# Kernel tuning notes

Hardware: AMD Instinct MI355X
Metric: run time of the kernel (lower is better)

Reference implementation:

```python
import jax, jax.numpy as jnp
import numpy as np

SEQLEN, K, OLDK, HEADS = 2048, 1024, 1024, 16
BASE = 10000.0


def rope(x):
    # x: [b, t, K]; RoPENd over 1 channel dim: rotate adjacent pairs
    # pair j at position t rotated by angle t * BASE**(-j/(K/2))
    t = x.shape[1]
    half = K // 2
    theta = 1.0 / (BASE ** (jnp.arange(half, dtype=jnp.float32) / half))  # [half]
    ang = jnp.arange(t, dtype=jnp.float32)[:, None] * theta[None, :]      # [t, half]
    cos, sin = jnp.cos(ang), jnp.sin(ang)
    xr = x.reshape(x.shape[0], t, half, 2)
    xe, xo = xr[..., 0], xr[..., 1]
    re = xe * cos - xo * sin
    im = xe * sin + xo * cos
    return jnp.stack([re, im], axis=-1).reshape(x.shape)


def setup_inputs() -> dict:
    key = jax.random.key(0)
    ks = jax.random.split(key, 5)
    b = 4
    x = jax.random.normal(ks[0], (b, SEQLEN, OLDK), jnp.float32)
    sc_in = 1.0 / np.sqrt(OLDK).astype(np.float32)
    Wq = jax.random.normal(ks[1], (K, OLDK), jnp.float32) * sc_in
    Wk = jax.random.normal(ks[2], (K, OLDK), jnp.float32) * sc_in
    Wv = jax.random.normal(ks[3], (K, OLDK), jnp.float32) * sc_in
    Wu = jax.random.normal(ks[4], (K, K), jnp.float32) * (1.0 / np.sqrt(K).astype(np.float32))
    bu = jnp.zeros((K,), jnp.float32)
    return {"x": x, "Wq": Wq, "Wk": Wk, "Wv": Wv, "Wu": Wu, "bu": bu}


def reference(x, Wq, Wk, Wv, Wu, bu):
    b, t, _ = x.shape
    h = HEADS
    s = K // h  # head dim
    q = rope(x @ Wq.T)   # [b, t, K]
    k = rope(x @ Wk.T)
    v = x @ Wv.T
    # split heads: [b, h, t, s]
    q = q.reshape(b, t, h, s).transpose(0, 2, 1, 3)
    k = k.reshape(b, t, h, s).transpose(0, 2, 1, 3)
    v = v.reshape(b, t, h, s).transpose(0, 2, 1, 3)
    dot = jnp.einsum('bhqd,bhkd->bhqk', q, k) / jnp.sqrt(jnp.float32(s))
    att = jax.nn.softmax(dot, axis=-1)
    out = jnp.einsum('bhqk,bhkd->bhqd', att, v)
    out = out.transpose(0, 2, 1, 3).reshape(b, t, h * s)
    return out @ Wu.T + bu
```

## Files before the change

kernel.cpp:

```cpp
#include <hip/hip_runtime.h>

#define TSEQ 2048
#define KDIM 1024
#define NHEAD 16
#define HDIM 64
#define BATCH 4
#define HALF 512

typedef __attribute__((ext_vector_type(4))) float f32x4;
typedef __attribute__((ext_vector_type(16))) float f32x16;
typedef __attribute__((ext_vector_type(8))) short short8;
typedef __attribute__((ext_vector_type(4))) unsigned short us4;
typedef __attribute__((ext_vector_type(4))) unsigned int u32x4;

#if __has_builtin(__builtin_amdgcn_exp2f)
#define EXP2(x) __builtin_amdgcn_exp2f(x)
#else
#define EXP2(x) __expf((x)*0.6931471805599453f)
#endif

__device__ __forceinline__ unsigned short f2bf(float f){
  unsigned int u = __float_as_uint(f);
  u += 0x7FFFu + ((u >> 16) & 1u);
  return (unsigned short)(u >> 16);
}

__device__ __forceinline__ unsigned int cvtpk(float a, float b){
  unsigned int r;
  asm("v_cvt_pk_bf16_f32 %0, %1, %2" : "=v"(r) : "v"(a), "v"(b));
  return r;
}

__device__ __forceinline__ f32x4 mfma16(short8 a, short8 b, f32x4 c){
  return __builtin_amdgcn_mfma_f32_16x16x32_bf16(a, b, c, 0, 0, 0);
}
__device__ __forceinline__ f32x16 mfma32(short8 a, short8 b, f32x16 c){
  return __builtin_amdgcn_mfma_f32_32x32x16_bf16(a, b, c, 0, 0, 0);
}

__device__ __forceinline__ void gl_lds16(const void* g, void* l){
  __builtin_amdgcn_global_load_lds(
      (const __attribute__((address_space(1))) unsigned int*)g,
      (__attribute__((address_space(3))) unsigned int*)l, 16, 0, 0);
}

__global__ __launch_bounds__(256) void cvt_bf16(const float* __restrict__ in,
                                                unsigned short* __restrict__ out,
                                                int n4){
  int i = blockIdx.x*256 + threadIdx.x;
  if (i >= n4) return;
  f32x4 v = ((const f32x4*)in)[i];
  us4 o;
  o[0] = f2bf(v[0]); o[1] = f2bf(v[1]); o[2] = f2bf(v[2]); o[3] = f2bf(v[3]);
  ((us4*)out)[i] = o;
}

__global__ __launch_bounds__(256) void trig_init(float2* __restrict__ csT){
  int idx = blockIdx.x*256 + threadIdx.x;
  int t = idx >> 9;
  int j = idx & (HALF-1);
  float theta = powf(10000.0f, -(float)j * (1.0f/(float)HALF));
  float ang = (float)t * theta;
  csT[idx] = make_float2(cosf(ang), sinf(ang));
}

__global__ __launch_bounds__(256) void gemm_qkv(
    const unsigned short* __restrict__ A,
    const unsigned short* __restrict__ Wq,
    const unsigned short* __restrict__ Wk,
    const unsigned short* __restrict__ Wv,
    unsigned short* __restrict__ Qo,
    unsigned short* __restrict__ Ko,
    unsigned short* __restrict__ Vo,
    const float2* __restrict__ csT){
  __shared__ __align__(16) unsigned short As[128*32];
  __shared__ __align__(16) unsigned short Bs[128*32];
  const int lin = blockIdx.y*64 + blockIdx.x;
  const int L = (lin & 7)*192 + (lin >> 3);
  const int bx = L/24, by = L%24;
  const int region = by >> 3;
  const int tm = bx*128, tn = (by & 7)*128;
  const unsigned short* Bw = region==0 ? Wq : (region==1 ? Wk : Wv);
  unsigned short* outp     = region==0 ? Qo : (region==1 ? Ko : Vo);
  const float scale = (region==0) ? 0.18033688011112042f : 1.0f;

  const int t  = threadIdx.x;
  const int w  = t>>6, l = t&63;
  const int wm = (w>>1)*64, wn = (w&1)*64;
  const int lr = l&15, g = l>>4, g4 = (l>>4)*4;

  f32x4 acc[4][4];
  #pragma unroll
  for (int i=0;i<4;i++)
    #pragma unroll
    for (int j=0;j<4;j++) acc[i][j] = (f32x4){0.f,0.f,0.f,0.f};

  const int sr = t>>2, cc = t&3;
  const int sc = (cc ^ ((sr>>1)&3))*8;
  const unsigned short* Ag = A  + (size_t)(tm+sr)*KDIM + sc;
  const unsigned short* Bg = Bw + (size_t)(tn+sr)*KDIM + sc;
  unsigned short* Al0 = As + t*8;
  unsigned short* Al1 = As + 2048 + t*8;
  unsigned short* Bl0 = Bs + t*8;
  unsigned short* Bl1 = Bs + 2048 + t*8;

  for (int k0=0; k0<KDIM; k0+=32){
    gl_lds16(Ag + k0, Al0);
    gl_lds16(Ag + (size_t)64*KDIM + k0, Al1);
    gl_lds16(Bg + k0, Bl0);
    gl_lds16(Bg + (size_t)64*KDIM + k0, Bl1);
    __syncthreads();
    short8 af[4], bfr[4];
    #pragma unroll
    for (int i=0;i<4;i++){
      int ra = wm+i*16+lr, rb = wn+i*16+lr;
      af[i]  = *(const short8*)&As[ra*32 + (g ^ ((ra>>1)&3))*8];
      bfr[i] = *(const short8*)&Bs[rb*32 + (g ^ ((rb>>1)&3))*8];
    }
    #pragma unroll
    for (int i=0;i<4;i++)
      #pragma unroll
      for (int j=0;j<4;j++)
        acc[i][j] = mfma16(af[i], bfr[j], acc[i][j]);
    __syncthreads();
  }

  #pragma unroll
  for (int i=0;i<4;i++){
    #pragma unroll
    for (int j=0;j<4;j++){
      #pragma unroll
      for (int r=0;r<4;r++){
        int row = tm + wm + i*16 + g4 + r;
        int col = tn + wn + j*16 + lr;
        float v = acc[i][j][r];
        if (region < 2){
          float pv = __shfl_xor(v, 1);
          int tp = row & (TSEQ-1);
          int jj = col >> 1;
          float2 cs = csT[tp*HALF + jj];
          float res = (col & 1) ? fmaf(pv, cs.y, v*cs.x)
                                : fmaf(v, cs.x, -(pv*cs.y));
          outp[(size_t)row*KDIM + col] = f2bf(res*scale);
        } else {
          outp[(size_t)row*KDIM + col] = f2bf(v);
        }
      }
    }
  }
}

__global__ __launch_bounds__(256) void gemm_out(
    const unsigned short* __restrict__ A,
    const unsigned short* __restrict__ Bw,
    float* __restrict__ outp,
    const float* __restrict__ bias){
  __shared__ __align__(16) unsigned short As[128*32];
  __shared__ __align__(16) unsigned short Bs[128*32];
  const int lin = blockIdx.y*64 + blockIdx.x;
  const int L = (lin & 7)*64 + (lin >> 3);
  const int bx = L>>3, by = L&7;
  const int tm = bx*128, tn = by*128;
  const int t  = threadIdx.x;
  const int w  = t>>6, l = t&63;
  const int wm = (w>>1)*64, wn = (w&1)*64;
  const int lr = l&15, g = l>>4, g4 = (l>>4)*4;

  f32x4 acc[4][4];
  #pragma unroll
  for (int i=0;i<4;i++)
    #pragma unroll
    for (int j=0;j<4;j++) acc[i][j] = (f32x4){0.f,0.f,0.f,0.f};

  const int sr = t>>2, cc = t&3;
  const int sc = (cc ^ ((sr>>1)&3))*8;
  const unsigned short* Ag = A  + (size_t)(tm+sr)*KDIM + sc;
  const unsigned short* Bg = Bw + (size_t)(tn+sr)*KDIM + sc;
  unsigned short* Al0 = As + t*8;
  unsigned short* Al1 = As + 2048 + t*8;
  unsigned short* Bl0 = Bs + t*8;
  unsigned short* Bl1 = Bs + 2048 + t*8;

  for (int k0=0; k0<KDIM; k0+=32){
    gl_lds16(Ag + k0, Al0);
    gl_lds16(Ag + (size_t)64*KDIM + k0, Al1);
    gl_lds16(Bg + k0, Bl0);
    gl_lds16(Bg + (size_t)64*KDIM + k0, Bl1);
    __syncthreads();
    short8 af[4], bfr[4];
    #pragma unroll
    for (int i=0;i<4;i++){
      int ra = wm+i*16+lr, rb = wn+i*16+lr;
      af[i]  = *(const short8*)&As[ra*32 + (g ^ ((ra>>1)&3))*8];
      bfr[i] = *(const short8*)&Bs[rb*32 + (g ^ ((rb>>1)&3))*8];
    }
    #pragma unroll
    for (int i=0;i<4;i++)
      #pragma unroll
      for (int j=0;j<4;j++)
        acc[i][j] = mfma16(af[i], bfr[j], acc[i][j]);
    __syncthreads();
  }

  #pragma unroll
  for (int i=0;i<4;i++){
    #pragma unroll
    for (int j=0;j<4;j++){
      #pragma unroll
      for (int r=0;r<4;r++){
        int row = tm + wm + i*16 + g4 + r;
        int col = tn + wn + j*16 + lr;
        outp[(size_t)row*KDIM + col] = acc[i][j][r] + bias[col];
      }
    }
  }
}

__global__ __launch_bounds__(256) void karr(const unsigned short* __restrict__ in,
                                            unsigned short* __restrict__ out){
  const int t = threadIdx.x;
  const int tl = blockIdx.x, h = blockIdx.y, b = blockIdx.z;
  const int ks = t>>6, l = t&63, ln = l&31, h2 = l>>5;
  short8 v = *(const short8*)&in[((size_t)b*TSEQ + tl*32 + ln)*KDIM + h*HDIM + ks*16 + h2*8];
  *(short8*)&out[(((size_t)(b*NHEAD + h)*64 + tl)*2048) + t*8] = v;
}

__global__ __launch_bounds__(256) void varr(const unsigned short* __restrict__ in,
                                            unsigned short* __restrict__ out){
  __shared__ __align__(16) unsigned short tile[32][72];
  const int t = threadIdx.x;
  const int tl = blockIdx.x, h = blockIdx.y, b = blockIdx.z;
  const int r = t>>3, c8 = (t&7)*8;
  short8 v = *(const short8*)&in[((size_t)b*TSEQ + tl*32 + r)*KDIM + h*HDIM + c8];
  *(short8*)&tile[r][c8] = v;
  __syncthreads();
  const int dt = t>>7, ks2 = (t>>6)&1;
  const int l = t&63, ln = l&31, h2 = l>>5;
  const int k0 = ks2*16 + h2*8, d = dt*32 + ln;
  unsigned short tmp[8];
  #pragma unroll
  for (int e=0;e<8;e++) tmp[e] = tile[k0+e][d];
  *(short8*)&out[(((size_t)(b*NHEAD + h)*64 + tl)*2048) + t*8] = *(const short8*)tmp;
}

__global__ __launch_bounds__(256, 4) void flash_attn4(
    const unsigned short* __restrict__ Q,
    const unsigned short* __restrict__ Kf,
    const unsigned short* __restrict__ Vf,
    unsigned short* __restrict__ Out){
  __shared__ __align__(16) unsigned short kv[3*4096];
  __shared__ __align__(16) float lbuf[4][32];
  const int t = threadIdx.x;
  const int w = t>>6, l = t&63;
  const int ln = l&31, h = l>>5;
  const int by = blockIdx.y;
  const int b = by>>4, hh = by&15;
  const int q0 = blockIdx.x*128 + w*32;
  const size_t bT = (size_t)b*TSEQ;
  const int hd0 = hh*HDIM;

  short8 qf[4];
  #pragma unroll
  for (int ks=0; ks<4; ks++)
    qf[ks] = *(const short8*)&Q[(bT + q0 + ln)*KDIM + hd0 + ks*16 + h*8];

  const unsigned short* tbK = Kf + (size_t)(b*NHEAD + hh)*64*2048;
  const unsigned short* tbV = Vf + (size_t)(b*NHEAD + hh)*64*2048;

  unsigned short* pA = kv;
  unsigned short* pB = kv + 4096;
  unsigned short* pC = kv + 8192;

  auto STG = [&](int tt, unsigned short* buf){
    gl_lds16(tbK + (size_t)tt*2048 + w*512 + l*8, buf + w*512);
    gl_lds16(tbV + (size_t)tt*2048 + w*512 + l*8, buf + 2048 + w*512);
  };

  STG(0, pA);
  STG(1, pB);
  asm volatile("s_waitcnt vmcnt(2)" ::: "memory");
  __builtin_amdgcn_s_barrier();

  f32x16 O0, O1;
  #pragma unroll
  for (int r=0;r<16;r++){ O0[r]=0.f; O1[r]=0.f; }
  float lsum = 0.f;

  for (int tt=0; tt<64; ++tt){
    if (tt < 62) STG(tt+2, pC);

    short8 kf0 = *(const short8*)&pA[0*512 + l*8];
    short8 kf1 = *(const short8*)&pA[1*512 + l*8];
    short8 kf2 = *(const short8*)&pA[2*512 + l*8];
    short8 kf3 = *(const short8*)&pA[3*512 + l*8];

    f32x16 S;
    #pragma unroll
    for (int r=0;r<16;r++) S[r]=0.f;
    __builtin_amdgcn_s_setprio(1);
    S = mfma32(kf0, qf[0], S);
    S = mfma32(kf1, qf[1], S);
    S = mfma32(kf2, qf[2], S);
    S = mfma32(kf3, qf[3], S);
    __builtin_amdgcn_s_setprio(0);

    float rs = 0.f;
    #pragma unroll
    for (int r=0;r<16;r++){ S[r] = EXP2(S[r]); rs += S[r]; }
    lsum += rs;

    unsigned int wds[8];
    #pragma unroll
    for (int i=0;i<8;i++) wds[i] = cvtpk(S[2*i], S[2*i+1]);

    unsigned int y0 = __shfl_xor(h ? wds[0] : wds[2], 32);
    unsigned int y1 = __shfl_xor(h ? wds[1] : wds[3], 32);
    unsigned int y2 = __shfl_xor(h ? wds[4] : wds[6], 32);
    unsigned int y3 = __shfl_xor(h ? wds[5] : wds[7], 32);

    u32x4 pw0 = h ? (u32x4){y0, y1, wds[2], wds[3]}
                  : (u32x4){wds[0], wds[1], y0, y1};
    u32x4 pw1 = h ? (u32x4){y2, y3, wds[6], wds[7]}
                  : (u32x4){wds[4], wds[5], y2, y3};
    short8 pa0 = *(short8*)&pw0;
    short8 pa1 = *(short8*)&pw1;

    short8 vf0 = *(const short8*)&pA[2048 + 0*512 + l*8];
    short8 vf1 = *(const short8*)&pA[2048 + 1*512 + l*8];
    short8 vf2 = *(const short8*)&pA[2048 + 2*512 + l*8];
    short8 vf3 = *(const short8*)&pA[2048 + 3*512 + l*8];
    __builtin_amdgcn_s_setprio(1);
    O0 = mfma32(pa0, vf0, O0);
    O0 = mfma32(pa1, vf1, O0);
    O1 = mfma32(pa0, vf2, O1);
    O1 = mfma32(pa1, vf3, O1);
    __builtin_amdgcn_s_setprio(0);

    if (tt < 62){
      asm volatile("s_waitcnt vmcnt(2)" ::: "memory");
    } else {
      asm volatile("s_waitcnt vmcnt(0)" ::: "memory");
    }
    __builtin_amdgcn_s_barrier();

    unsigned short* tp = pA; pA = pB; pB = pC; pC = tp;
  }

  float lfull = lsum + __shfl_xor(lsum, 32);
  float linv = 1.0f / lfull;
  if (h == 0) lbuf[w][ln] = linv;
  __syncthreads();

  #pragma unroll
  for (int gg=0; gg<4; gg++){
    f32x4 lv = *(const f32x4*)&lbuf[w][gg*8 + h*4];
    #pragma unroll
    for (int i=0; i<4; i++){
      int r = gg*4 + i;
      int row = q0 + gg*8 + h*4 + i;
      size_t base = (bT + row)*KDIM + hd0;
      Out[base + ln]      = f2bf(O0[r]*lv[i]);
      Out[base + 32 + ln] = f2bf(O1[r]*lv[i]);
    }
  }
}

extern "C" void kernel_launch(void* const* d_in, const int* in_sizes, int n_in,
                              void* d_out, int out_size, void* d_ws, size_t ws_size,
                              hipStream_t stream){
  (void)in_sizes; (void)n_in; (void)out_size; (void)ws_size;
  const float* x  = (const float*)d_in[0];
  const float* Wq = (const float*)d_in[1];
  const float* Wk = (const float*)d_in[2];
  const float* Wv = (const float*)d_in[3];
  const float* Wu = (const float*)d_in[4];
  const float* bu = (const float*)d_in[5];

  char* ws = (char*)d_ws;
  size_t off = 0;
  auto alloc = [&](size_t bytes){ void* p = ws + off; off += bytes; return p; };
  unsigned short* xb  = (unsigned short*)alloc(16777216);
  unsigned short* qb  = (unsigned short*)alloc(16777216);
  unsigned short* kb  = (unsigned short*)alloc(16777216);
  unsigned short* vb  = (unsigned short*)alloc(16777216);
  unsigned short* kfr = (unsigned short*)alloc(16777216);
  unsigned short* wqb = (unsigned short*)alloc(2097152);
  unsigned short* wkb = (unsigned short*)alloc(2097152);
  unsigned short* wvb = (unsigned short*)alloc(2097152);
  unsigned short* wub = (unsigned short*)alloc(2097152);
  float2* csT = (float2*)alloc(8388608);
  unsigned short* vfr = kb;
  unsigned short* att = xb;

  cvt_bf16<<<8192, 256, 0, stream>>>(x,  xb,  2097152);
  cvt_bf16<<<1024, 256, 0, stream>>>(Wq, wqb, 262144);
  cvt_bf16<<<1024, 256, 0, stream>>>(Wk, wkb, 262144);
  cvt_bf16<<<1024, 256, 0, stream>>>(Wv, wvb, 262144);
  cvt_bf16<<<1024, 256, 0, stream>>>(Wu, wub, 262144);
  trig_init<<<4096, 256, 0, stream>>>(csT);

  gemm_qkv<<<dim3(64,24), 256, 0, stream>>>(xb, wqb, wkb, wvb,
                                            qb, kb, vb, csT);

  karr<<<dim3(64,16,4), 256, 0, stream>>>(kb, kfr);
  varr<<<dim3(64,16,4), 256, 0, stream>>>(vb, vfr);
  flash_attn4<<<dim3(16,64), 256, 0, stream>>>(qb, kfr, vfr, att);
  gemm_out<<<dim3(64,8), 256, 0, stream>>>(att, wub, (float*)d_out, bu);
}
```

Baseline: 364.5 us.

## Triple-buffer LDS staging in QKV GEMM to overlap global loads with MFMA

Replaces the single-buffer load/sync/compute loop in the QKV projection GEMM with a three-stage LDS ring. Tile k+2 is prefetched while tile k is computed, using vmcnt waits and raw barriers instead of two __syncthreads per iteration. The aim is to hide global-to-LDS latency behind MFMA work. In exchange LDS use triples, which may lower occupancy, and correctness depends on the manual waitcnt counts and the ordering of the buffer rotation.

```diff
diff --git a/kernel.cpp b/kernel.cpp
--- a/kernel.cpp
+++ b/kernel.cpp
@@ -73,8 +73,7 @@
     unsigned short* __restrict__ Ko,
     unsigned short* __restrict__ Vo,
     const float2* __restrict__ csT){
-  __shared__ __align__(16) unsigned short As[128*32];
-  __shared__ __align__(16) unsigned short Bs[128*32];
+  __shared__ __align__(16) unsigned short kv[3*8192];
   const int lin = blockIdx.y*64 + blockIdx.x;
   const int L = (lin & 7)*192 + (lin >> 3);
   const int bx = L/24, by = L%24;
@@ -99,30 +98,48 @@
   const int sc = (cc ^ ((sr>>1)&3))*8;
   const unsigned short* Ag = A  + (size_t)(tm+sr)*KDIM + sc;
   const unsigned short* Bg = Bw + (size_t)(tn+sr)*KDIM + sc;
-  unsigned short* Al0 = As + t*8;
-  unsigned short* Al1 = As + 2048 + t*8;
-  unsigned short* Bl0 = Bs + t*8;
-  unsigned short* Bl1 = Bs + 2048 + t*8;
-
-  for (int k0=0; k0<KDIM; k0+=32){
-    gl_lds16(Ag + k0, Al0);
-    gl_lds16(Ag + (size_t)64*KDIM + k0, Al1);
-    gl_lds16(Bg + k0, Bl0);
-    gl_lds16(Bg + (size_t)64*KDIM + k0, Bl1);
-    __syncthreads();
+
+  unsigned short* b0 = kv;
+  unsigned short* b1 = kv + 8192;
+  unsigned short* b2 = kv + 16384;
+
+  auto STG = [&](int k, unsigned short* buf){
+    const int k0 = k*32;
+    gl_lds16(Ag + k0, buf + t*8);
+    gl_lds16(Ag + (size_t)64*KDIM + k0, buf + 2048 + t*8);
+    gl_lds16(Bg + k0, buf + 4096 + t*8);
+    gl_lds16(Bg + (size_t)64*KDIM + k0, buf + 4096 + 2048 + t*8);
+  };
+
+  STG(0, b0);
+  STG(1, b1);
+  asm volatile("s_waitcnt vmcnt(4)" ::: "memory");
+  __builtin_amdgcn_s_barrier();
+
+  for (int k=0; k<32; ++k){
+    if (k < 30) STG(k+2, b2);
+
     short8 af[4], bfr[4];
     #pragma unroll
     for (int i=0;i<4;i++){
       int ra = wm+i*16+lr, rb = wn+i*16+lr;
-      af[i]  = *(const short8*)&As[ra*32 + (g ^ ((ra>>1)&3))*8];
-      bfr[i] = *(const short8*)&Bs[rb*32 + (g ^ ((rb>>1)&3))*8];
+      af[i]  = *(const short8*)&b0[ra*32 + (g ^ ((ra>>1)&3))*8];
+      bfr[i] = *(const short8*)&b0[4096 + rb*32 + (g ^ ((rb>>1)&3))*8];
     }
     #pragma unroll
     for (int i=0;i<4;i++)
       #pragma unroll
       for (int j=0;j<4;j++)
         acc[i][j] = mfma16(af[i], bfr[j], acc[i][j]);
-    __syncthreads();
+
+    if (k < 30){
+      asm volatile("s_waitcnt vmcnt(4)" ::: "memory");
+      __builtin_amdgcn_s_barrier();
+    } else if (k == 30){
+      asm volatile("s_waitcnt vmcnt(0)" ::: "memory");
+      __builtin_amdgcn_s_barrier();
+    }
+    unsigned short* tp = b0; b0 = b1; b1 = b2; b2 = tp;
   }
 
   #pragma unroll
```

New measurement: 340.8 us. 6.5% less time.
